# Kernel optimization log

Measured on AMD Instinct MI355X. Metric: run time of the kernel, lower is better.

## Reference

```python
import jax, jax.numpy as jnp
import numpy as np

B = 4            # scenes
N = 100000       # points per scene
BN = B * N
M = 200000       # occupied target voxels
C_IMG = 64       # img_feat_dim
C_3D = 32        # INIT_DIM (3D feature width at p1 scale)
COORD_MAX = 256  # voxel grid extent per axis


def setup_inputs() -> dict:
    key = jax.random.key(0)
    k1, k2, k3, k4, k5, k6 = jax.random.split(key, 6)
    # batched voxel coords: col0 = batch idx, cols1:4 = xyz voxel coords
    bcol = jax.random.randint(k1, (M, 1), 0, B, dtype=jnp.int32)
    xyz = jax.random.randint(k2, (M, 3), 0, COORD_MAX, dtype=jnp.int32)
    tgt_coords = jnp.concatenate([bcol, xyz], axis=1)  # (M,4)
    # each point maps onto some target voxel (torch code asserts full validity)
    pts_idx = jax.random.randint(k3, (BN,), 0, M, dtype=jnp.int32)
    pfeat = jax.random.normal(k4, (BN, C_IMG), dtype=jnp.float32)
    tgt_feats = jax.random.normal(k5, (M, C_3D), dtype=jnp.float32)
    W_fuse = jax.random.normal(k6, (C_3D + C_IMG, C_3D), dtype=jnp.float32) * 0.05
    b_fuse = jnp.zeros((C_3D,), dtype=jnp.float32)
    return {"pfeat": pfeat, "tgt_feats": tgt_feats, "W_fuse": W_fuse,
            "b_fuse": b_fuse, "tgt_coords": tgt_coords, "pts_idx": pts_idx}


def reference(pfeat, tgt_feats, W_fuse, b_fuse, tgt_coords, pts_idx):
    # point voxel coords (stride-snapped in torch; identity here since points map to voxels)
    pts_coords = tgt_coords[pts_idx]                              # (BN,4)
    # --- key packing (mirrors _pack_keys with shift-to-nonnegative) ---
    xyz_all = jnp.concatenate([pts_coords[:, 1:], tgt_coords[:, 1:]], axis=0)
    shift = jnp.maximum(-xyz_all.min(axis=0), 0)
    pts_xyz = pts_coords[:, 1:] + shift
    tgt_xyz = tgt_coords[:, 1:] + shift
    max_xyz = jnp.maximum(pts_xyz.max(axis=0), tgt_xyz.max(axis=0))
    mx, my, mz = max_xyz[0] + 1, max_xyz[1] + 1, max_xyz[2] + 1

    def pack(b, xyz):
        return ((b * mx + xyz[:, 0]) * my + xyz[:, 1]) * mz + xyz[:, 2]

    pts_key = pack(pts_coords[:, 0], pts_xyz)                     # (BN,)
    tgt_key = pack(tgt_coords[:, 0], tgt_xyz)                     # (M,)
    # --- sort target keys, binary-search point keys (torch.sort + searchsorted) ---
    order = jnp.argsort(tgt_key)
    tgt_key_sorted = tgt_key[order]
    pos = jnp.minimum(jnp.searchsorted(tgt_key_sorted, pts_key), M - 1)
    tgt_idx = order[pos]                                          # (BN,) voxel each point lands in
    # --- scatter-mean of 2D point features into voxels (_scatter_mean) ---
    sums = jax.ops.segment_sum(pfeat, tgt_idx, num_segments=M)    # (M,C_IMG)
    cnt = jax.ops.segment_sum(jnp.ones((pfeat.shape[0], 1), pfeat.dtype),
                              tgt_idx, num_segments=M)            # (M,1)
    img_feat_u = sums / jnp.maximum(cnt, 1.0)
    # --- ME.cat + 1x1 MinkowskiConvolution fuse == concat + matmul ---
    fused = jnp.concatenate([tgt_feats, img_feat_u], axis=1)      # (M, C_3D+C_IMG)
    return fused @ W_fuse + b_fuse                                # (M, C_3D)
```

## Files before the change

kernel.cpp:

```cpp
#include <hip/hip_runtime.h>

#define HBITS 19
#define HSIZE (1u << HBITS)
#define HMASK (HSIZE - 1u)
#define EMPTY_KEY 0xFFFFFFFFu
#define SLOTS 8

__device__ __forceinline__ unsigned hash_key(unsigned k) {
    return (k * 2654435761u) >> (32 - HBITS);
}

__device__ __forceinline__ unsigned pack_key(int4 c) {
    return ((unsigned)c.x << 24) | ((unsigned)c.y << 16) |
           ((unsigned)c.z << 8) | (unsigned)c.w;
}

__global__ __launch_bounds__(256)
void build_hash(const int4* __restrict__ tgt_coords, int M,
                uint2* __restrict__ htab) {
    int v = blockIdx.x * blockDim.x + threadIdx.x;
    if (v >= M) return;
    unsigned key = pack_key(tgt_coords[v]);
    unsigned h = hash_key(key);
    while (true) {
        unsigned prev = atomicCAS(&htab[h].x, EMPTY_KEY, key);
        if (prev == EMPTY_KEY || prev == key) {
            atomicMin(&htab[h].y, (unsigned)v);
            break;
        }
        h = (h + 1u) & HMASK;
    }
}

__global__ __launch_bounds__(256)
void fill_slots(const int* __restrict__ pts_idx,
                const int4* __restrict__ tgt_coords,
                const uint2* __restrict__ htab,
                int BN,
                int* __restrict__ cnt,
                int* __restrict__ slotbuf,
                int* __restrict__ ohead,
                int* __restrict__ nxt) {
    int p = blockIdx.x * blockDim.x + threadIdx.x;
    if (p >= BN) return;
    int vox = pts_idx[p];
    unsigned key = pack_key(tgt_coords[vox]);
    unsigned h = hash_key(key);
    uint2 e = htab[h];
    while (e.x != key) { h = (h + 1u) & HMASK; e = htab[h]; }
    int c = (int)e.y;
    int idx = atomicAdd(&cnt[c], 1) + 1;
    if (idx < SLOTS) slotbuf[c * SLOTS + idx] = p;
    else             nxt[p] = atomicExch(&ohead[c], p);
}

#define VPB 8
__global__ __launch_bounds__(256)
void gather_fuse(const float2* __restrict__ pf2,
                 const float* __restrict__ tgtf,
                 const int* __restrict__ cnt,
                 const int4* __restrict__ slot4,
                 const int* __restrict__ ohead,
                 const int* __restrict__ nxt,
                 const float* __restrict__ W,
                 const float* __restrict__ bias,
                 int M,
                 float* __restrict__ out) {
    __shared__ __align__(16) float xs[VPB][104];

    int t = threadIdx.x;
    int grp = t >> 5;
    int g   = t & 31;
    int v = blockIdx.x * VPB + grp;
    bool valid = (v < M);

    if (valid) {
        int n = cnt[v] + 1;
        int4 sa = make_int4(0, 0, 0, 0), sb = make_int4(0, 0, 0, 0);
        if (n > 0) sa = slot4[(size_t)v * 2];
        if (n > 4) sb = slot4[(size_t)v * 2 + 1];
        float2 f0 = {0,0}, f1 = {0,0}, f2 = {0,0}, f3 = {0,0};
        float2 f4 = {0,0}, f5 = {0,0}, f6 = {0,0}, f7 = {0,0};
        if (n > 0) f0 = pf2[(size_t)sa.x * 32 + g];
        if (n > 1) f1 = pf2[(size_t)sa.y * 32 + g];
        if (n > 2) f2 = pf2[(size_t)sa.z * 32 + g];
        if (n > 3) f3 = pf2[(size_t)sa.w * 32 + g];
        if (n > 4) f4 = pf2[(size_t)sb.x * 32 + g];
        if (n > 5) f5 = pf2[(size_t)sb.y * 32 + g];
        if (n > 6) f6 = pf2[(size_t)sb.z * 32 + g];
        if (n > 7) f7 = pf2[(size_t)sb.w * 32 + g];
        float sx = ((f0.x + f1.x) + (f2.x + f3.x)) + ((f4.x + f5.x) + (f6.x + f7.x));
        float sy = ((f0.y + f1.y) + (f2.y + f3.y)) + ((f4.y + f5.y) + (f6.y + f7.y));
        if (n > SLOTS) {
            int p = ohead[v];
            while (p >= 0) {
                float2 f = pf2[(size_t)p * 32 + g];
                sx += f.x; sy += f.y;
                p = nxt[p];
            }
        }
        float inv = 1.0f / fmaxf((float)n, 1.0f);
        xs[grp][g] = tgtf[(size_t)v * 32 + g];
        *reinterpret_cast<float2*>(&xs[grp][32 + 2 * g]) =
            make_float2(sx * inv, sy * inv);
    }

    float wcol[96];
#pragma unroll
    for (int k = 0; k < 96; ++k) wcol[k] = W[k * 32 + g];

    __syncthreads();

    if (valid) {
        float acc = bias[g];
#pragma unroll
        for (int k4 = 0; k4 < 24; ++k4) {
            float4 x = *reinterpret_cast<const float4*>(&xs[grp][k4 * 4]);
            acc = fmaf(x.x, wcol[4 * k4 + 0], acc);
            acc = fmaf(x.y, wcol[4 * k4 + 1], acc);
            acc = fmaf(x.z, wcol[4 * k4 + 2], acc);
            acc = fmaf(x.w, wcol[4 * k4 + 3], acc);
        }
        out[(size_t)v * 32 + g] = acc;
    }
}

extern "C" void kernel_launch(void* const* d_in, const int* in_sizes, int n_in,
                              void* d_out, int out_size, void* d_ws, size_t ws_size,
                              hipStream_t stream) {
    const float* pfeat      = (const float*)d_in[0];
    const float* tgt_feats  = (const float*)d_in[1];
    const float* W_fuse     = (const float*)d_in[2];
    const float* b_fuse     = (const float*)d_in[3];
    const int*   tgt_coords = (const int*)d_in[4];
    const int*   pts_idx    = (const int*)d_in[5];
    float* out = (float*)d_out;

    const int M  = in_sizes[4] / 4;
    const int BN = in_sizes[5];

    char* ws = (char*)d_ws;
    uint2* htab    = (uint2*)ws;
    size_t off = (size_t)HSIZE * 8;
    int*   cnt     = (int*)(ws + off);              off += (size_t)M * 4;
    int*   ohead   = (int*)(ws + off);              off += (size_t)M * 4;
    int*   slotbuf = (int*)(ws + off);              off += (size_t)M * SLOTS * 4;
    int*   nxt     = (int*)(ws + off);

    size_t ff_bytes = (size_t)HSIZE * 8 + (size_t)M * 8;
    hipMemsetAsync(htab, 0xFF, ff_bytes, stream);

    const int TB = 256;
    build_hash<<<(M + TB - 1) / TB, TB, 0, stream>>>(
        (const int4*)tgt_coords, M, htab);
    fill_slots<<<(BN + TB - 1) / TB, TB, 0, stream>>>(
        pts_idx, (const int4*)tgt_coords, htab, BN, cnt, slotbuf, ohead, nxt);
    gather_fuse<<<(M + VPB - 1) / VPB, TB, 0, stream>>>(
        (const float2*)pfeat, tgt_feats, cnt, (const int4*)slotbuf, ohead, nxt,
        W_fuse, b_fuse, M, out);
}
```

Measured before the change: 313.4 us.

## Precompute canonical voxel per target and tile the fuse matmul across 128 voxels

Adds a canonize kernel that resolves each target voxel's hash lookup once, so fill_slots becomes a single indexed load per point instead of repeating a hash probe. The gather_fuse kernel now stages 128 voxels per block in shared memory and does the 96x32 matmul with each thread computing 16 outputs for one voxel. The wave-uniform weights are read through scalar loads instead of 96 per-thread registers. This cuts redundant hash probes and weight loads at the cost of an extra kernel launch, a larger shared-memory tile, and fewer blocks in the gather stage.

```diff
diff --git a/kernel.cpp b/kernel.cpp
--- a/kernel.cpp
+++ b/kernel.cpp
@@ -33,9 +33,21 @@
 }
 
 __global__ __launch_bounds__(256)
+void canonize(const int4* __restrict__ tgt_coords,
+              const uint2* __restrict__ htab, int M,
+              int* __restrict__ canon) {
+    int v = blockIdx.x * blockDim.x + threadIdx.x;
+    if (v >= M) return;
+    unsigned key = pack_key(tgt_coords[v]);
+    unsigned h = hash_key(key);
+    uint2 e = htab[h];
+    while (e.x != key) { h = (h + 1u) & HMASK; e = htab[h]; }
+    canon[v] = (int)e.y;
+}
+
+__global__ __launch_bounds__(256)
 void fill_slots(const int* __restrict__ pts_idx,
-                const int4* __restrict__ tgt_coords,
-                const uint2* __restrict__ htab,
+                const int* __restrict__ canon,
                 int BN,
                 int* __restrict__ cnt,
                 int* __restrict__ slotbuf,
@@ -43,18 +55,14 @@
                 int* __restrict__ nxt) {
     int p = blockIdx.x * blockDim.x + threadIdx.x;
     if (p >= BN) return;
-    int vox = pts_idx[p];
-    unsigned key = pack_key(tgt_coords[vox]);
-    unsigned h = hash_key(key);
-    uint2 e = htab[h];
-    while (e.x != key) { h = (h + 1u) & HMASK; e = htab[h]; }
-    int c = (int)e.y;
+    int c = canon[pts_idx[p]];
     int idx = atomicAdd(&cnt[c], 1) + 1;
     if (idx < SLOTS) slotbuf[c * SLOTS + idx] = p;
     else             nxt[p] = atomicExch(&ohead[c], p);
 }
 
-#define VPB 8
+#define VOXB 128
+#define XSTR 98
 __global__ __launch_bounds__(256)
 void gather_fuse(const float2* __restrict__ pf2,
                  const float* __restrict__ tgtf,
@@ -66,62 +74,80 @@
                  const float* __restrict__ bias,
                  int M,
                  float* __restrict__ out) {
-    __shared__ __align__(16) float xs[VPB][104];
+    __shared__ __align__(16) float xs[VOXB][XSTR];
 
     int t = threadIdx.x;
     int grp = t >> 5;
     int g   = t & 31;
-    int v = blockIdx.x * VPB + grp;
-    bool valid = (v < M);
+    int vbase = blockIdx.x * VOXB;
 
-    if (valid) {
-        int n = cnt[v] + 1;
-        int4 sa = make_int4(0, 0, 0, 0), sb = make_int4(0, 0, 0, 0);
-        if (n > 0) sa = slot4[(size_t)v * 2];
-        if (n > 4) sb = slot4[(size_t)v * 2 + 1];
-        float2 f0 = {0,0}, f1 = {0,0}, f2 = {0,0}, f3 = {0,0};
-        float2 f4 = {0,0}, f5 = {0,0}, f6 = {0,0}, f7 = {0,0};
-        if (n > 0) f0 = pf2[(size_t)sa.x * 32 + g];
-        if (n > 1) f1 = pf2[(size_t)sa.y * 32 + g];
-        if (n > 2) f2 = pf2[(size_t)sa.z * 32 + g];
-        if (n > 3) f3 = pf2[(size_t)sa.w * 32 + g];
-        if (n > 4) f4 = pf2[(size_t)sb.x * 32 + g];
-        if (n > 5) f5 = pf2[(size_t)sb.y * 32 + g];
-        if (n > 6) f6 = pf2[(size_t)sb.z * 32 + g];
-        if (n > 7) f7 = pf2[(size_t)sb.w * 32 + g];
-        float sx = ((f0.x + f1.x) + (f2.x + f3.x)) + ((f4.x + f5.x) + (f6.x + f7.x));
-        float sy = ((f0.y + f1.y) + (f2.y + f3.y)) + ((f4.y + f5.y) + (f6.y + f7.y));
-        if (n > SLOTS) {
-            int p = ohead[v];
-            while (p >= 0) {
-                float2 f = pf2[(size_t)p * 32 + g];
-                sx += f.x; sy += f.y;
-                p = nxt[p];
+    for (int pp = 0; pp < VOXB / 8; ++pp) {
+        int vb = pp * 8 + grp;
+        int v  = vbase + vb;
+        if (v < M) {
+            int n = cnt[v] + 1;
+            int4 sa = make_int4(0, 0, 0, 0), sb = make_int4(0, 0, 0, 0);
+            if (n > 0) sa = slot4[(size_t)v * 2];
+            if (n > 4) sb = slot4[(size_t)v * 2 + 1];
+            float2 f0 = {0,0}, f1 = {0,0}, f2 = {0,0}, f3 = {0,0};
+            float2 f4 = {0,0}, f5 = {0,0}, f6 = {0,0}, f7 = {0,0};
+            if (n > 0) f0 = pf2[(size_t)sa.x * 32 + g];
+            if (n > 1) f1 = pf2[(size_t)sa.y * 32 + g];
+            if (n > 2) f2 = pf2[(size_t)sa.z * 32 + g];
+            if (n > 3) f3 = pf2[(size_t)sa.w * 32 + g];
+            if (n > 4) f4 = pf2[(size_t)sb.x * 32 + g];
+            if (n > 5) f5 = pf2[(size_t)sb.y * 32 + g];
+            if (n > 6) f6 = pf2[(size_t)sb.z * 32 + g];
+            if (n > 7) f7 = pf2[(size_t)sb.w * 32 + g];
+            float sx = ((f0.x + f1.x) + (f2.x + f3.x)) + ((f4.x + f5.x) + (f6.x + f7.x));
+            float sy = ((f0.y + f1.y) + (f2.y + f3.y)) + ((f4.y + f5.y) + (f6.y + f7.y));
+            if (n > SLOTS) {
+                int p = ohead[v];
+                while (p >= 0) {
+                    float2 f = pf2[(size_t)p * 32 + g];
+                    sx += f.x; sy += f.y;
+                    p = nxt[p];
+                }
             }
+            float inv = 1.0f / fmaxf((float)n, 1.0f);
+            xs[vb][g] = tgtf[(size_t)v * 32 + g];
+            *reinterpret_cast<float2*>(&xs[vb][32 + 2 * g]) =
+                make_float2(sx * inv, sy * inv);
         }
-        float inv = 1.0f / fmaxf((float)n, 1.0f);
-        xs[grp][g] = tgtf[(size_t)v * 32 + g];
-        *reinterpret_cast<float2*>(&xs[grp][32 + 2 * g]) =
-            make_float2(sx * inv, sy * inv);
     }
-
-    float wcol[96];
-#pragma unroll
-    for (int k = 0; k < 96; ++k) wcol[k] = W[k * 32 + g];
 
     __syncthreads();
 
-    if (valid) {
-        float acc = bias[g];
+    int vb2 = t & (VOXB - 1);
+    int ocb = __builtin_amdgcn_readfirstlane((t >> 7) << 4);
+    int v2  = vbase + vb2;
+    if (v2 < M) {
+        float acc[16];
 #pragma unroll
+        for (int j = 0; j < 16; ++j) acc[j] = bias[ocb + j];
+
+#pragma unroll 4
         for (int k4 = 0; k4 < 24; ++k4) {
-            float4 x = *reinterpret_cast<const float4*>(&xs[grp][k4 * 4]);
-            acc = fmaf(x.x, wcol[4 * k4 + 0], acc);
-            acc = fmaf(x.y, wcol[4 * k4 + 1], acc);
-            acc = fmaf(x.z, wcol[4 * k4 + 2], acc);
-            acc = fmaf(x.w, wcol[4 * k4 + 3], acc);
+            float2 xa = *reinterpret_cast<const float2*>(&xs[vb2][k4 * 4]);
+            float2 xb = *reinterpret_cast<const float2*>(&xs[vb2][k4 * 4 + 2]);
+            const float* w0 = W + (k4 * 4 + 0) * 32 + ocb;
+            const float* w1 = W + (k4 * 4 + 1) * 32 + ocb;
+            const float* w2 = W + (k4 * 4 + 2) * 32 + ocb;
+            const float* w3 = W + (k4 * 4 + 3) * 32 + ocb;
+#pragma unroll
+            for (int j = 0; j < 16; ++j) {
+                acc[j] = fmaf(xa.x, w0[j], acc[j]);
+                acc[j] = fmaf(xa.y, w1[j], acc[j]);
+                acc[j] = fmaf(xb.x, w2[j], acc[j]);
+                acc[j] = fmaf(xb.y, w3[j], acc[j]);
+            }
         }
-        out[(size_t)v * 32 + g] = acc;
+
+        float4* o = reinterpret_cast<float4*>(out + (size_t)v2 * 32 + ocb);
+#pragma unroll
+        for (int q = 0; q < 4; ++q)
+            o[q] = make_float4(acc[4 * q], acc[4 * q + 1],
+                               acc[4 * q + 2], acc[4 * q + 3]);
     }
 }
 
@@ -144,6 +170,7 @@
     size_t off = (size_t)HSIZE * 8;
     int*   cnt     = (int*)(ws + off);              off += (size_t)M * 4;
     int*   ohead   = (int*)(ws + off);              off += (size_t)M * 4;
+    int*   canon   = (int*)(ws + off);              off += (size_t)M * 4;
     int*   slotbuf = (int*)(ws + off);              off += (size_t)M * SLOTS * 4;
     int*   nxt     = (int*)(ws + off);
 
@@ -153,9 +180,11 @@
     const int TB = 256;
     build_hash<<<(M + TB - 1) / TB, TB, 0, stream>>>(
         (const int4*)tgt_coords, M, htab);
+    canonize<<<(M + TB - 1) / TB, TB, 0, stream>>>(
+        (const int4*)tgt_coords, htab, M, canon);
     fill_slots<<<(BN + TB - 1) / TB, TB, 0, stream>>>(
-        pts_idx, (const int4*)tgt_coords, htab, BN, cnt, slotbuf, ohead, nxt);
-    gather_fuse<<<(M + VPB - 1) / VPB, TB, 0, stream>>>(
+        pts_idx, canon, BN, cnt, slotbuf, ohead, nxt);
+    gather_fuse<<<(M + VOXB - 1) / VOXB, TB, 0, stream>>>(
         (const float2*)pfeat, tgt_feats, cnt, (const int4*)slotbuf, ohead, nxt,
         W_fuse, b_fuse, M, out);
 }
```

Result: slower. 323.2 us (+3.1%).
